# Optimization experiments

Measured on AMD Instinct MI355X. Metric: run time of the kernel, lower is better.

The kernel has to match this reference:

```python
import jax, jax.numpy as jnp
import numpy as np

TOP_K = 8  # config.top_k


def setup_inputs() -> dict:
    key = jax.random.key(0)
    k1, k2 = jax.random.split(key)
    B, S, H, E = 4, 4096, 4096, 64
    x = jax.random.normal(k1, (B, S, H), dtype=jnp.float32)
    # nn.Linear(hidden_size, expert_num, bias=False) weight: [E, H]
    W = jax.random.normal(k2, (E, H), dtype=jnp.float32) / np.sqrt(H).astype(np.float32)
    return {"x": x, "W": W}


def reference(x, W):
    # gate linear: [B,S,H] @ [E,H]^T -> [B,S,E]
    logits = jnp.einsum('bsh,eh->bse', x, W)
    # top-k along experts
    topk_vals, indices = jax.lax.top_k(logits, TOP_K)  # [B,S,K]
    # scatter topk values into a -inf-filled tensor. Since the scattered src
    # values are exactly the logits at those indices, this equals masking.
    E = logits.shape[-1]
    mask = jax.nn.one_hot(indices, E, dtype=bool).any(axis=-2)  # [B,S,E]
    sparse_logits = jnp.where(mask, logits, -jnp.inf)
    sparse_probs = jax.nn.softmax(sparse_logits, axis=-1)  # [B,S,E]
    gate_logit = logits.reshape(-1, E)  # [B*S, E]
    return sparse_probs, indices, gate_logit
```

## Files before the change

kernel.cpp:

```cpp
#include <hip/hip_runtime.h>
#include <math.h>

#define H_DIM  4096
#define E_NUM  64
#define N_TOK  16384
#define TPB    64
#define KC     64
#define NCHUNK (H_DIM / KC)
#define TOPK   8

#define N_PROBS  (N_TOK * E_NUM)
#define N_IDX    (N_TOK * TOPK)
#define OFF_IDX  N_PROBS
#define OFF_GATE (N_PROBS + N_IDX)

__global__ __launch_bounds__(256, 1)
void gating_kernel(const float* __restrict__ x, const float* __restrict__ W,
                   float* __restrict__ out) {
  __shared__ union {
    float xs[2][KC][TPB];
    float lg[TPB][E_NUM + 1];
  } u;
  __shared__ float ws[2][KC][E_NUM];

  const int tid  = threadIdx.x;
  const int tok0 = blockIdx.x * TPB;
  const int tx   = tid & 15;
  const int ty   = tid >> 4;

  const float* xg = x + (size_t)tok0 * H_DIM;

  float4 xr[4], wr[4];

  auto gload = [&](int kb) {
#pragma unroll
    for (int p = 0; p < 4; ++p) {
      const int f4  = tid + 256 * p;
      const int row = f4 & 63;
      const int kq  = f4 >> 6;
      xr[p] = *(const float4*)(xg + row * H_DIM + kb + 4 * kq);
      wr[p] = *(const float4*)(W  + row * H_DIM + kb + 4 * kq);
    }
  };
  auto sstore = [&](int b) {
#pragma unroll
    for (int p = 0; p < 4; ++p) {
      const int f4  = tid + 256 * p;
      const int row = f4 & 63;
      const int k0  = (f4 >> 6) << 2;
      u.xs[b][k0 + 0][row] = xr[p].x;
      u.xs[b][k0 + 1][row] = xr[p].y;
      u.xs[b][k0 + 2][row] = xr[p].z;
      u.xs[b][k0 + 3][row] = xr[p].w;
      ws[b][k0 + 0][row] = wr[p].x;
      ws[b][k0 + 1][row] = wr[p].y;
      ws[b][k0 + 2][row] = wr[p].z;
      ws[b][k0 + 3][row] = wr[p].w;
    }
  };

  gload(0);
  sstore(0);
  __syncthreads();

  double accd[4][4];
#pragma unroll
  for (int i = 0; i < 4; ++i)
#pragma unroll
    for (int j = 0; j < 4; ++j) accd[i][j] = 0.0;

  for (int c = 0; c < NCHUNK; ++c) {
    if (c + 1 < NCHUNK) gload((c + 1) * KC);
    const int b = c & 1;

    float ca[4][4];
#pragma unroll
    for (int i = 0; i < 4; ++i)
#pragma unroll
      for (int j = 0; j < 4; ++j) ca[i][j] = 0.f;

#pragma unroll 8
    for (int k = 0; k < KC; ++k) {
      const float4 av = *(const float4*)&u.xs[b][k][4 * ty];
      const float4 bv = *(const float4*)&ws[b][k][4 * tx];
      const float a[4]  = {av.x, av.y, av.z, av.w};
      const float bb[4] = {bv.x, bv.y, bv.z, bv.w};
#pragma unroll
      for (int i = 0; i < 4; ++i)
#pragma unroll
        for (int j = 0; j < 4; ++j)
          ca[i][j] = fmaf(a[i], bb[j], ca[i][j]);
    }
#pragma unroll
    for (int i = 0; i < 4; ++i)
#pragma unroll
      for (int j = 0; j < 4; ++j) accd[i][j] += (double)ca[i][j];

    if (c + 1 < NCHUNK) {
      sstore((c + 1) & 1);
      __syncthreads();
    }
  }

  float acc[4][4];
#pragma unroll
  for (int i = 0; i < 4; ++i)
#pragma unroll
    for (int j = 0; j < 4; ++j) acc[i][j] = (float)accd[i][j];

  float* gate = out + OFF_GATE;
#pragma unroll
  for (int i = 0; i < 4; ++i) {
    const int t = 4 * ty + i;
    float4 v = make_float4(acc[i][0], acc[i][1], acc[i][2], acc[i][3]);
    *(float4*)(gate + (size_t)(tok0 + t) * E_NUM + 4 * tx) = v;
  }

  __syncthreads();
#pragma unroll
  for (int i = 0; i < 4; ++i)
#pragma unroll
    for (int j = 0; j < 4; ++j)
      u.lg[4 * ty + i][4 * tx + j] = acc[i][j];
  __syncthreads();

  if (tid < TPB) {
    const int t = tid;
    float vals[TOPK];
    int   idxs[TOPK];
#pragma unroll
    for (int p = 0; p < TOPK; ++p) {
      float best = -INFINITY;
      int   bi   = 0;
      for (int e = 0; e < E_NUM; ++e) {
        const float v = u.lg[t][e];
        if (v > best) { best = v; bi = e; }
      }
      vals[p] = best;
      idxs[p] = bi;
      u.lg[t][bi] = -INFINITY;
    }
    const float m = vals[0];
    float s = 0.f, pr[TOPK];
#pragma unroll
    for (int p = 0; p < TOPK; ++p) { pr[p] = __expf(vals[p] - m); s += pr[p]; }
    const float inv = 1.0f / s;
    for (int e = 0; e < E_NUM; ++e) u.lg[t][e] = 0.f;
#pragma unroll
    for (int p = 0; p < TOPK; ++p) u.lg[t][idxs[p]] = pr[p] * inv;

    float* oidx = out + OFF_IDX + (size_t)(tok0 + t) * TOPK;
#pragma unroll
    for (int p = 0; p < TOPK; ++p) oidx[p] = (float)idxs[p];
  }
  __syncthreads();

  float* oprob = out + (size_t)tok0 * E_NUM;
#pragma unroll
  for (int p = 0; p < 16; ++p) {
    const int f = tid + 256 * p;
    oprob[f] = u.lg[f >> 6][f & 63];
  }
}

extern "C" void kernel_launch(void* const* d_in, const int* in_sizes, int n_in,
                              void* d_out, int out_size, void* d_ws, size_t ws_size,
                              hipStream_t stream) {
  const float* x = (const float*)d_in[0];
  const float* W = (const float*)d_in[1];
  float* out = (float*)d_out;
  dim3 grid(N_TOK / TPB);
  dim3 block(256);
  gating_kernel<<<grid, block, 0, stream>>>(x, W, out);
}
```

Measured before the change: 453.3 us.

## Split the K dimension across waves with a per-lane token GEMV and uniform W loads

Replaces the LDS-tiled 64x64 GEMM with a scheme where each lane owns one token and each of the four waves handles a 1024-wide slice of the hidden dimension. W addresses are wave-uniform, so they can be served by scalar loads and broadcast to all lanes, and LDS staging and the per-chunk barriers go away. The four partial sums per token are then reduced through shared memory in double precision. The cost is uncoalesced per-lane row reads of x, very high register pressure from 64 double accumulators, and low occupancy, which may leave memory latency poorly hidden.

```diff
diff --git a/kernel.cpp b/kernel.cpp
--- a/kernel.cpp
+++ b/kernel.cpp
@@ -4,162 +4,141 @@
 #define H_DIM  4096
 #define E_NUM  64
 #define N_TOK  16384
-#define TPB    64
-#define KC     64
-#define NCHUNK (H_DIM / KC)
 #define TOPK   8
+#define KSEG   1024
+#define NCH    16
 
 #define N_PROBS  (N_TOK * E_NUM)
-#define N_IDX    (N_TOK * TOPK)
 #define OFF_IDX  N_PROBS
-#define OFF_GATE (N_PROBS + N_IDX)
+#define OFF_GATE (N_PROBS + N_TOK * TOPK)
 
 __global__ __launch_bounds__(256, 1)
 void gating_kernel(const float* __restrict__ x, const float* __restrict__ W,
                    float* __restrict__ out) {
-  __shared__ union {
-    float xs[2][KC][TPB];
-    float lg[TPB][E_NUM + 1];
-  } u;
-  __shared__ float ws[2][KC][E_NUM];
+  __shared__ float ps[4][E_NUM][64];
 
-  const int tid  = threadIdx.x;
-  const int tok0 = blockIdx.x * TPB;
-  const int tx   = tid & 15;
-  const int ty   = tid >> 4;
+  const int tid   = threadIdx.x;
+  const int lane  = tid & 63;
+  const int wv    = __builtin_amdgcn_readfirstlane(tid >> 6);
+  const int tok0  = blockIdx.x * 64;
+  const int kbase = wv * KSEG;
 
-  const float* xg = x + (size_t)tok0 * H_DIM;
+  const float* __restrict__ xrow = x + (size_t)(tok0 + lane) * H_DIM + kbase;
+  const float* __restrict__ wseg = W + kbase;
 
-  float4 xr[4], wr[4];
+  double acc64[E_NUM];
+#pragma unroll
+  for (int e = 0; e < E_NUM; ++e) acc64[e] = 0.0;
 
-  auto gload = [&](int kb) {
+  float4 cur[4];
 #pragma unroll
-    for (int p = 0; p < 4; ++p) {
-      const int f4  = tid + 256 * p;
-      const int row = f4 & 63;
-      const int kq  = f4 >> 6;
-      xr[p] = *(const float4*)(xg + row * H_DIM + kb + 4 * kq);
-      wr[p] = *(const float4*)(W  + row * H_DIM + kb + 4 * kq);
+  for (int q = 0; q < 4; ++q) cur[q] = *(const float4*)(xrow + 4 * q);
+
+#pragma unroll 1
+  for (int c = 0; c < NCH; ++c) {
+    float ca[E_NUM];
+#pragma unroll
+    for (int e = 0; e < E_NUM; ++e) ca[e] = 0.f;
+
+#pragma unroll 1
+    for (int s = 0; s < 4; ++s) {
+      const int i = 4 * c + s;
+
+      float4 use[4];
+#pragma unroll
+      for (int q = 0; q < 4; ++q) use[q] = cur[q];
+
+      int ni = i + 1; if (ni > 63) ni = 63;
+#pragma unroll
+      for (int q = 0; q < 4; ++q)
+        cur[q] = *(const float4*)(xrow + 16 * ni + 4 * q);
+
+      const float xk[16] = {use[0].x, use[0].y, use[0].z, use[0].w,
+                            use[1].x, use[1].y, use[1].z, use[1].w,
+                            use[2].x, use[2].y, use[2].z, use[2].w,
+                            use[3].x, use[3].y, use[3].z, use[3].w};
+
+#pragma unroll
+      for (int e0 = 0; e0 < E_NUM; e0 += 4) {
+#pragma unroll
+        for (int j = 0; j < 4; ++j) {
+          const float* wp = wseg + (size_t)(e0 + j) * H_DIM + 16 * i;
+#pragma unroll
+          for (int q = 0; q < 4; ++q) {
+            const float4 wq = *(const float4*)(wp + 4 * q);
+            ca[e0 + j] = fmaf(xk[4 * q + 0], wq.x, ca[e0 + j]);
+            ca[e0 + j] = fmaf(xk[4 * q + 1], wq.y, ca[e0 + j]);
+            ca[e0 + j] = fmaf(xk[4 * q + 2], wq.z, ca[e0 + j]);
+            ca[e0 + j] = fmaf(xk[4 * q + 3], wq.w, ca[e0 + j]);
+          }
+        }
+      }
     }
-  };
-  auto sstore = [&](int b) {
+
 #pragma unroll
-    for (int p = 0; p < 4; ++p) {
-      const int f4  = tid + 256 * p;
-      const int row = f4 & 63;
-      const int k0  = (f4 >> 6) << 2;
-      u.xs[b][k0 + 0][row] = xr[p].x;
-      u.xs[b][k0 + 1][row] = xr[p].y;
-      u.xs[b][k0 + 2][row] = xr[p].z;
-      u.xs[b][k0 + 3][row] = xr[p].w;
-      ws[b][k0 + 0][row] = wr[p].x;
-      ws[b][k0 + 1][row] = wr[p].y;
-      ws[b][k0 + 2][row] = wr[p].z;
-      ws[b][k0 + 3][row] = wr[p].w;
-    }
-  };
+    for (int e = 0; e < E_NUM; ++e) acc64[e] += (double)ca[e];
+  }
 
-  gload(0);
-  sstore(0);
+#pragma unroll
+  for (int e = 0; e < E_NUM; ++e) ps[wv][e][lane] = (float)acc64[e];
   __syncthreads();
 
-  double accd[4][4];
 #pragma unroll
-  for (int i = 0; i < 4; ++i)
+  for (int p = 0; p < 16; ++p) {
+    const int f = tid + 256 * p;
+    const int t = f & 63;
+    const int e = f >> 6;
+    double v = 0.0;
 #pragma unroll
-    for (int j = 0; j < 4; ++j) accd[i][j] = 0.0;
-
-  for (int c = 0; c < NCHUNK; ++c) {
-    if (c + 1 < NCHUNK) gload((c + 1) * KC);
-    const int b = c & 1;
-
-    float ca[4][4];
-#pragma unroll
-    for (int i = 0; i < 4; ++i)
-#pragma unroll
-      for (int j = 0; j < 4; ++j) ca[i][j] = 0.f;
-
-#pragma unroll 8
-    for (int k = 0; k < KC; ++k) {
-      const float4 av = *(const float4*)&u.xs[b][k][4 * ty];
-      const float4 bv = *(const float4*)&ws[b][k][4 * tx];
-      const float a[4]  = {av.x, av.y, av.z, av.w};
-      const float bb[4] = {bv.x, bv.y, bv.z, bv.w};
-#pragma unroll
-      for (int i = 0; i < 4; ++i)
-#pragma unroll
-        for (int j = 0; j < 4; ++j)
-          ca[i][j] = fmaf(a[i], bb[j], ca[i][j]);
-    }
-#pragma unroll
-    for (int i = 0; i < 4; ++i)
-#pragma unroll
-      for (int j = 0; j < 4; ++j) accd[i][j] += (double)ca[i][j];
-
-    if (c + 1 < NCHUNK) {
-      sstore((c + 1) & 1);
-      __syncthreads();
-    }
+    for (int s = 0; s < 4; ++s) v += (double)ps[s][e][t];
+    ps[0][e][t] = (float)v;
   }
-
-  float acc[4][4];
-#pragma unroll
-  for (int i = 0; i < 4; ++i)
-#pragma unroll
-    for (int j = 0; j < 4; ++j) acc[i][j] = (float)accd[i][j];
-
-  float* gate = out + OFF_GATE;
-#pragma unroll
-  for (int i = 0; i < 4; ++i) {
-    const int t = 4 * ty + i;
-    float4 v = make_float4(acc[i][0], acc[i][1], acc[i][2], acc[i][3]);
-    *(float4*)(gate + (size_t)(tok0 + t) * E_NUM + 4 * tx) = v;
-  }
-
-  __syncthreads();
-#pragma unroll
-  for (int i = 0; i < 4; ++i)
-#pragma unroll
-    for (int j = 0; j < 4; ++j)
-      u.lg[4 * ty + i][4 * tx + j] = acc[i][j];
   __syncthreads();
 
-  if (tid < TPB) {
+  float* __restrict__ gate = out + OFF_GATE;
+#pragma unroll
+  for (int p = 0; p < 16; ++p) {
+    const int g = tid + 256 * p;
+    gate[(size_t)tok0 * E_NUM + g] = ps[0][g & 63][g >> 6];
+  }
+  __syncthreads();
+
+  if (tid < 64) {
     const int t = tid;
     float vals[TOPK];
     int   idxs[TOPK];
 #pragma unroll
-    for (int p = 0; p < TOPK; ++p) {
+    for (int r = 0; r < TOPK; ++r) {
       float best = -INFINITY;
       int   bi   = 0;
       for (int e = 0; e < E_NUM; ++e) {
-        const float v = u.lg[t][e];
+        const float v = ps[0][e][t];
         if (v > best) { best = v; bi = e; }
       }
-      vals[p] = best;
-      idxs[p] = bi;
-      u.lg[t][bi] = -INFINITY;
+      vals[r] = best;
+      idxs[r] = bi;
+      ps[0][bi][t] = -INFINITY;
     }
     const float m = vals[0];
-    float s = 0.f, pr[TOPK];
+    float ssum = 0.f, pr[TOPK];
 #pragma unroll
-    for (int p = 0; p < TOPK; ++p) { pr[p] = __expf(vals[p] - m); s += pr[p]; }
-    const float inv = 1.0f / s;
-    for (int e = 0; e < E_NUM; ++e) u.lg[t][e] = 0.f;
+    for (int r = 0; r < TOPK; ++r) { pr[r] = __expf(vals[r] - m); ssum += pr[r]; }
+    const float inv = 1.0f / ssum;
+    for (int e = 0; e < E_NUM; ++e) ps[0][e][t] = 0.f;
 #pragma unroll
-    for (int p = 0; p < TOPK; ++p) u.lg[t][idxs[p]] = pr[p] * inv;
+    for (int r = 0; r < TOPK; ++r) ps[0][idxs[r]][t] = pr[r] * inv;
 
-    float* oidx = out + OFF_IDX + (size_t)(tok0 + t) * TOPK;
+    float* __restrict__ oidx = out + OFF_IDX + (size_t)(tok0 + t) * TOPK;
 #pragma unroll
-    for (int p = 0; p < TOPK; ++p) oidx[p] = (float)idxs[p];
+    for (int r = 0; r < TOPK; ++r) oidx[r] = (float)idxs[r];
   }
   __syncthreads();
 
-  float* oprob = out + (size_t)tok0 * E_NUM;
+  float* __restrict__ oprob = out + (size_t)tok0 * E_NUM;
 #pragma unroll
   for (int p = 0; p < 16; ++p) {
-    const int f = tid + 256 * p;
-    oprob[f] = u.lg[f >> 6][f & 63];
+    const int g = tid + 256 * p;
+    oprob[g] = ps[0][g & 63][g >> 6];
   }
 }
 
@@ -169,7 +148,5 @@
   const float* x = (const float*)d_in[0];
   const float* W = (const float*)d_in[1];
   float* out = (float*)d_out;
-  dim3 grid(N_TOK / TPB);
-  dim3 block(256);
-  gating_kernel<<<grid, block, 0, stream>>>(x, W, out);
+  gating_kernel<<<dim3(N_TOK / 64), dim3(256), 0, stream>>>(x, W, out);
 }
```

Measured after the change: 1.673 ms. 3.69x slower.
